# Kernel optimization log

Hardware: AMD Instinct MI355X
Metric: run time of the kernel (lower is better)

The kernel has to match this reference:

```python
import jax, jax.numpy as jnp
import numpy as np
from jax import lax

N_ITER = 50  # entmax-bisect iterations (entmax library default)
DEG = 12    # neighbors per node in global item graph


def entmax_bisect(X, alpha):
    # entmax with per-row alpha, over axis=1. X: [B, L, 1], alpha: [B, 1, 1]
    d = X.shape[1]
    Xa = X * (alpha - 1.0)
    inv = 1.0 / (alpha - 1.0)
    _p = lambda z: jnp.maximum(z, 0.0) ** inv
    max_val = jnp.max(Xa, axis=1, keepdims=True)
    tau_lo = max_val - 1.0                                   # _gp(1, alpha) = 1
    tau_hi = max_val - jnp.power(1.0 / d, alpha - 1.0)       # _gp(1/d, alpha)
    f_lo = jnp.sum(_p(Xa - tau_lo), axis=1, keepdims=True) - 1.0

    def body(i, carry):
        tau_lo, dm, _ = carry
        dm = dm * 0.5
        tau_m = tau_lo + dm
        f_m = jnp.sum(_p(Xa - tau_m), axis=1, keepdims=True) - 1.0
        tau_lo = jnp.where(f_m * f_lo >= 0.0, tau_m, tau_lo)
        return (tau_lo, dm, tau_m)

    tau_lo, dm, tau_m = lax.fori_loop(0, N_ITER, body, (tau_lo, tau_hi - tau_lo, tau_lo))
    p_m = _p(Xa - tau_m)
    return p_m / jnp.sum(p_m, axis=1, keepdims=True)  # ensure_sum_one


def setup_inputs() -> dict:
    key = jax.random.key(0)
    ks = jax.random.split(key, 10)
    B, L, D, N = 1024, 50, 256, 40000
    E = N * DEG
    stdv = 1.0 / np.sqrt(D)
    u = lambda k, shape: jax.random.uniform(k, shape, jnp.float32, -stdv, stdv)

    item_emb = u(ks[0], (N, D)).at[0].set(0.0)  # padding_idx=0
    items = jax.random.randint(ks[1], (B, L), 0, N)
    inputs_seq = jax.random.randint(ks[2], (B, L), 0, N)
    alias_inputs = jax.random.randint(ks[3], (B, L), 0, L)
    target_embedding = jax.random.normal(ks[4], (B, 1, 2 * D), jnp.float32)

    # sparse global item adjacency (row-normalized, DEG neighbors per node)
    adj_rows = jnp.repeat(jnp.arange(N, dtype=jnp.int32), DEG)
    adj_cols = jax.random.randint(ks[5], (E,), 0, N, dtype=jnp.int32)
    adj_vals = jax.random.uniform(ks[6], (E,), jnp.float32) / DEG

    kp = jax.random.split(ks[7], 10)
    return {
        "items": items, "inputs_seq": inputs_seq, "alias_inputs": alias_inputs,
        "target_embedding": target_embedding, "item_emb": item_emb,
        "adj_rows": adj_rows, "adj_cols": adj_cols, "adj_vals": adj_vals,
        "wf_w": u(kp[0], (D, 2 * D)), "wf_b": u(kp[1], (D,)),
        "alphaw_w": u(kp[2], (1, D)), "alphaw_b": u(kp[3], (1,)),
        "at_w0": u(kp[4], (1, D)), "at_w1": u(kp[5], (D, D)),
        "at_w2": u(kp[6], (D, D)), "at_bias": u(kp[7], (D,)),
    }


def reference(items, inputs_seq, alias_inputs, target_embedding, item_emb,
              adj_rows, adj_cols, adj_vals, wf_w, wf_b, alphaw_w, alphaw_b,
              at_w0, at_w1, at_w2, at_bias):
    N = item_emb.shape[0]
    # GlobalItemConv (1 layer): h = (x + adj @ x) / 2 via sparse SpMM
    agg = jax.ops.segment_sum(adj_vals[:, None] * item_emb[adj_cols], adj_rows,
                              num_segments=N)
    graph_embs = (item_emb + agg) * 0.5

    hidden = graph_embs[items]                              # [B, L, D] (dropout: eval)
    target_emb = target_embedding @ wf_w.T + wf_b           # [B, 1, D]

    # get_alpha: sigmoid + 1, then masked_fill(==1 -> 1.00001)
    alpha_ent = jax.nn.sigmoid(target_emb @ alphaw_w.T + alphaw_b) + 1.0  # [B,1,1]
    alpha_ent = jnp.where(alpha_ent == 1.0, 1.00001, alpha_ent)

    # tglobal_attention
    scores = jax.nn.relu(hidden @ at_w1 + target_emb @ at_w2 + at_bias) @ at_w0.T  # [B,L,1]
    attn = entmax_bisect(scores, alpha_ent)                 # sparse softmax over L
    c = jnp.einsum('blo,bld->bod', attn, hidden)[:, 0, :]   # alpha^T @ v, squeeze -> [B,D]

    c = jax.nn.selu(c)
    return c / jnp.linalg.norm(c, axis=-1, keepdims=True)
```

## Files before the change

kernel.cpp:

```cpp
#include <hip/hip_runtime.h>
#include <hip/hip_bf16.h>
#include <math.h>

#define BB 1024
#define LL 50
#define DD 256
#define TWO_D 512
#define NN 40000
#define DEG 12
#define NITER 50

typedef __attribute__((ext_vector_type(8))) short short8;
typedef __attribute__((ext_vector_type(4))) float floatx4;

__device__ __forceinline__ float wave_sum64(float v) {
#pragma unroll
    for (int off = 32; off > 0; off >>= 1) v += __shfl_xor(v, off, 64);
    return v;
}
__device__ __forceinline__ float wave_max64(float v) {
#pragma unroll
    for (int off = 32; off > 0; off >>= 1) v = fmaxf(v, __shfl_xor(v, off, 64));
    return v;
}
__device__ __forceinline__ float dpp_sum64(float v) {
#define DPPADD(ctrl, rm, bm) \
    v += __int_as_float(__builtin_amdgcn_update_dpp(0, __float_as_int(v), ctrl, rm, bm, true))
    DPPADD(0x111, 0xF, 0xF);
    DPPADD(0x112, 0xF, 0xF);
    DPPADD(0x114, 0xF, 0xE);
    DPPADD(0x118, 0xF, 0xC);
    DPPADD(0x142, 0xA, 0xF);
    DPPADD(0x143, 0xC, 0xF);
#undef DPPADD
    return __int_as_float(__builtin_amdgcn_readlane(__float_as_int(v), 63));
}
__device__ __forceinline__ float bf2f(ushort u) {
    union { unsigned int i; float f; } c; c.i = ((unsigned int)u) << 16; return c.f;
}
__device__ __forceinline__ ushort f2bf(float f) {
    __hip_bfloat16 h = __float2bfloat16(f);
    return *(ushort*)&h;
}
__device__ __forceinline__ float hw_exp2(float x) { return __builtin_amdgcn_exp2f(x); }
__device__ __forceinline__ float hw_log2(float x) { return __builtin_amdgcn_logf(x); }

__global__ __launch_bounds__(256) void k_stage1(
    const float* __restrict__ emb, ushort* __restrict__ ebf,
    const int* __restrict__ items, int* __restrict__ flags,
    const float* __restrict__ wf_w, const float* __restrict__ wf_b,
    const float* __restrict__ at_w2, const float* __restrict__ at_bias,
    const float* __restrict__ aw, const float* __restrict__ ab,
    const float* __restrict__ at_w1,
    float* __restrict__ Wc, float* __restrict__ v,
    float* __restrict__ bc, float* __restrict__ c0,
    ushort* __restrict__ w1t)
{
    __shared__ float wcol[DD];
    __shared__ float4 s_p[4][64];
    __shared__ float wred[4];
    __shared__ ushort s_t[4][DD];
    int bid = blockIdx.x;
    int tid = threadIdx.x;

    if (bid < 512) {
        int k = bid;
        int lane = tid & 63, wv = tid >> 6;
        int ng = tid & 63;
        int dq = tid >> 6;

        wcol[tid] = wf_w[tid * TWO_D + k];
        __syncthreads();

        float4 acc = {0.f, 0.f, 0.f, 0.f};
        const float4* w24 = (const float4*)at_w2;
#pragma unroll 8
        for (int d = dq * 64; d < dq * 64 + 64; ++d) {
            float4 w2 = w24[d * 64 + ng];
            float wc = wcol[d];
            acc.x += wc * w2.x; acc.y += wc * w2.y;
            acc.z += wc * w2.z; acc.w += wc * w2.w;
        }
        s_p[dq][ng] = acc;

        float s1 = wcol[tid] * aw[tid];
        s1 = wave_sum64(s1);
        if (lane == 0) wred[wv] = s1;
        __syncthreads();
        if (tid == 0) v[k] = wred[0] + wred[1] + wred[2] + wred[3];

        if (tid < 64) {
            float4 r0 = s_p[0][tid], r1 = s_p[1][tid];
            float4 r2 = s_p[2][tid], r3 = s_p[3][tid];
            float4 rr;
            rr.x = (r0.x + r1.x) + (r2.x + r3.x);
            rr.y = (r0.y + r1.y) + (r2.y + r3.y);
            rr.z = (r0.z + r1.z) + (r2.z + r3.z);
            rr.w = (r0.w + r1.w) + (r2.w + r3.w);
            *(float4*)(Wc + k * DD + tid * 4) = rr;
        }

        if (k < 64) {
            int k0 = k * 4;
#pragma unroll
            for (int j = 0; j < 4; ++j)
                s_t[j][tid] = f2bf(at_w1[(k0 + j) * DD + tid]);
            __syncthreads();
            ushort4 pk;
            pk.x = s_t[0][tid]; pk.y = s_t[1][tid];
            pk.z = s_t[2][tid]; pk.w = s_t[3][tid];
            *(ushort4*)(w1t + tid * DD + k0) = pk;
        }

        if (k == 0) {
            __syncthreads();
            wcol[tid] = wf_b[tid];
            __syncthreads();
            float b[8];
#pragma unroll
            for (int j = 0; j < 8; ++j) b[j] = 0.f;
#pragma unroll 4
            for (int d = 0; d < DD; d += 8) {
#pragma unroll
                for (int j = 0; j < 8; ++j)
                    b[j] += wcol[d + j] * at_w2[(d + j) * DD + tid];
            }
            bc[tid] = at_bias[tid] + ((b[0] + b[1]) + (b[2] + b[3]))
                                   + ((b[4] + b[5]) + (b[6] + b[7]));
            float s2 = wcol[tid] * aw[tid];
            s2 = wave_sum64(s2);
            if (lane == 0) wred[wv] = s2;
            __syncthreads();
            if (tid == 0) c0[0] = wred[0] + wred[1] + wred[2] + wred[3] + ab[0];
        }
    } else if (bid < 712) {
        int i = (bid - 512) * 256 + tid;
        flags[items[i]] = 1;
    } else {
        int base4 = (bid - 712) * (256 * 8) + tid;
        float4 val[8];
#pragma unroll
        for (int j = 0; j < 8; ++j)
            val[j] = *(const float4*)(emb + (size_t)(base4 + j * 256) * 4);
#pragma unroll
        for (int j = 0; j < 8; ++j) {
            ushort4 o;
            o.x = f2bf(val[j].x); o.y = f2bf(val[j].y);
            o.z = f2bf(val[j].z); o.w = f2bf(val[j].w);
            *(ushort4*)(ebf + (size_t)(base4 + j * 256) * 4) = o;
        }
    }
}

__global__ __launch_bounds__(256) void k_stage2(
    const ushort* __restrict__ ebf, const int* __restrict__ adj_cols,
    const float* __restrict__ adj_vals, const int* __restrict__ flags,
    ushort* __restrict__ gbf,
    const float* __restrict__ tgt, const float* __restrict__ Wc,
    const float* __restrict__ bc, const float* __restrict__ v,
    const float* __restrict__ c0, float* __restrict__ t2,
    float* __restrict__ alpha)
{
    __shared__ float x_s[4 * TWO_D];
    int bid = blockIdx.x;
    int tid = threadIdx.x;
    int wv = tid >> 6, lane = tid & 63;

    if (bid < 1024) {
        int t = bid;
        int btile = t >> 2, ntile = t & 3;
        int b0 = btile * 4, n0 = ntile * 64;
        int j = wv;
        for (int i = tid; i < 4 * TWO_D; i += 256) x_s[i] = tgt[b0 * TWO_D + i];
        __syncthreads();

        float acc = bc[n0 + lane];
        const float* xr = x_s + j * TWO_D;
#pragma unroll 8
        for (int k = 0; k < TWO_D; ++k)
            acc += xr[k] * Wc[k * DD + n0 + lane];
        t2[(b0 + j) * DD + n0 + lane] = acc;

        if (ntile == 0) {
            float s = 0.f;
#pragma unroll
            for (int i = 0; i < 8; ++i) s += xr[lane + 64 * i] * v[lane + 64 * i];
            s = wave_sum64(s);
            if (lane == 0) {
                float a = 1.f + 1.f / (1.f + expf(-(s + c0[0])));
                if (a == 1.f) a = 1.00001f;
                alpha[b0 + j] = a;
            }
        }
    } else {
        int n = (bid - 1024) * 4 + wv;
        if (flags[n] != 1) return;
        int colv = 0; float valv = 0.f;
        if (lane < DEG) { colv = adj_cols[n * DEG + lane]; valv = adj_vals[n * DEG + lane]; }
        int cols[DEG]; float vals[DEG];
#pragma unroll
        for (int k = 0; k < DEG; ++k) {
            cols[k] = __builtin_amdgcn_readlane(colv, k);
            vals[k] = __int_as_float(__builtin_amdgcn_readlane(__float_as_int(valv), k));
        }
        ushort4 s = *(const ushort4*)(ebf + (size_t)n * DD + lane * 4);
        ushort4 e[DEG];
#pragma unroll
        for (int k = 0; k < DEG; ++k)
            e[k] = *(const ushort4*)(ebf + (size_t)cols[k] * DD + lane * 4);
        float a0 = bf2f(s.x), a1 = bf2f(s.y), a2 = bf2f(s.z), a3 = bf2f(s.w);
#pragma unroll
        for (int k = 0; k < DEG; ++k) {
            float vv = vals[k];
            a0 += vv * bf2f(e[k].x); a1 += vv * bf2f(e[k].y);
            a2 += vv * bf2f(e[k].z); a3 += vv * bf2f(e[k].w);
        }
        ushort4 o;
        o.x = f2bf(0.5f * a0); o.y = f2bf(0.5f * a1);
        o.z = f2bf(0.5f * a2); o.w = f2bf(0.5f * a3);
        *(ushort4*)(gbf + (size_t)n * DD + lane * 4) = o;
    }
}

__device__ __forceinline__ float pw(float z, float invv) {
    return hw_exp2(invv * hw_log2(z));
}

#define SA_LD 264

__global__ __launch_bounds__(256, 2) void k_fused(
    const int* __restrict__ items, const ushort* __restrict__ gbf,
    const ushort* __restrict__ w1t, const float* __restrict__ t2,
    const float* __restrict__ at_w0, const float* __restrict__ alpha,
    float* __restrict__ out)
{
    __shared__ __align__(16) ushort sA[64 * SA_LD];
    __shared__ __align__(16) ushort sB[256 * 72];
    __shared__ float t2_s[DD];
    __shared__ float sred[64][4];
    __shared__ float scores_s[64];
    __shared__ int s_items[64];
    __shared__ float attn_s[64];
    __shared__ float red[4];

    int b = blockIdx.x;
    int tid = threadIdx.x;
    int lane = tid & 63, wv = tid >> 6;
    int cn = lane & 15, q = lane >> 4;
    int n0 = wv * 64;

    if (tid < 64) {
        int l = (tid < LL) ? tid : 0;
        s_items[tid] = items[b * LL + l];
    }
    t2_s[tid] = t2[b * DD + tid];
    __syncthreads();

#pragma unroll
    for (int it = 0; it < 8; ++it) {
        int i = tid + it * 256;
        int row = i >> 5, ch = i & 31;
        *(uint4*)(sA + row * SA_LD + ch * 8) =
            *(const uint4*)(gbf + (size_t)s_items[row] * DD + ch * 8);
    }

    floatx4 acc[4][4];
#pragma unroll
    for (int mt = 0; mt < 4; ++mt)
#pragma unroll
        for (int nt = 0; nt < 4; ++nt)
            acc[mt][nt] = (floatx4){0.f, 0.f, 0.f, 0.f};

#pragma unroll 1
    for (int kc = 0; kc < 4; ++kc) {
#pragma unroll
        for (int it = 0; it < 8; ++it) {
            int i = tid + it * 256;
            int n = i >> 3, seg = i & 7;
            *(uint4*)(sB + n * 72 + seg * 8) =
                *(const uint4*)(w1t + n * DD + kc * 64 + seg * 8);
        }
        __syncthreads();
#pragma unroll
        for (int ks = 0; ks < 2; ++ks) {
            short8 af[4], bfr[4];
#pragma unroll
            for (int mt = 0; mt < 4; ++mt)
                af[mt] = *(const short8*)(sA + (mt * 16 + cn) * SA_LD + kc * 64 + ks * 32 + q * 8);
#pragma unroll
            for (int nt = 0; nt < 4; ++nt)
                bfr[nt] = *(const short8*)(sB + (n0 + nt * 16 + cn) * 72 + ks * 32 + q * 8);
#pragma unroll
            for (int mt = 0; mt < 4; ++mt)
#pragma unroll
                for (int nt = 0; nt < 4; ++nt)
                    acc[mt][nt] = __builtin_amdgcn_mfma_f32_16x16x32_bf16(
                        af[mt], bfr[nt], acc[mt][nt], 0, 0, 0);
        }
        __syncthreads();
    }

    float w0v[4];
#pragma unroll
    for (int nt = 0; nt < 4; ++nt) w0v[nt] = at_w0[n0 + nt * 16 + cn];
#pragma unroll
    for (int mt = 0; mt < 4; ++mt) {
#pragma unroll
        for (int r = 0; r < 4; ++r) {
            int row = mt * 16 + q * 4 + r;
            float p = 0.f;
#pragma unroll
            for (int nt = 0; nt < 4; ++nt) {
                int col = n0 + nt * 16 + cn;
                float vvv = acc[mt][nt][r] + t2_s[col];
                p += fmaxf(vvv, 0.f) * w0v[nt];
            }
            p += __shfl_xor(p, 1, 64);
            p += __shfl_xor(p, 2, 64);
            p += __shfl_xor(p, 4, 64);
            p += __shfl_xor(p, 8, 64);
            if (cn == 0) sred[row][wv] = p;
        }
    }
    __syncthreads();
    if (tid < 64)
        scores_s[tid] = sred[tid][0] + sred[tid][1] + sred[tid][2] + sred[tid][3];
    __syncthreads();

    if (tid < 64) {
        int l = tid;
        float a = alpha[b];
        float am1 = a - 1.f;
        float invv = 1.f / am1;
        float x = (l < LL) ? scores_s[l] : -__builtin_inff();
        float Xa = x * am1;

        float mx = wave_max64(Xa);
        float tau_lo = mx - 1.f;
        float tau_hi = mx - hw_exp2(am1 * hw_log2(1.f / (float)LL));

        float f_lo = dpp_sum64(pw(fmaxf(Xa - tau_lo, 0.f), invv)) - 1.f;

        float dm = tau_hi - tau_lo;
        float tau_m = tau_lo;
#pragma unroll 1
        for (int it = 0; it < NITER; ++it) {
            dm *= 0.5f;
            tau_m = tau_lo + dm;
            if (tau_m == tau_lo) break;
            float f_m = dpp_sum64(pw(fmaxf(Xa - tau_m, 0.f), invv)) - 1.f;
            if (f_m * f_lo >= 0.f) tau_lo = tau_m;
        }
        float pm = pw(fmaxf(Xa - tau_m, 0.f), invv);
        float s = dpp_sum64(pm);
        if (l < LL) attn_s[l] = pm / s;
    }
    __syncthreads();

    int d = tid;
    float c0_ = 0.f, c1_ = 0.f;
#pragma unroll
    for (int l = 0; l < LL; l += 2) {
        c0_ += attn_s[l]     * bf2f(sA[l * SA_LD + d]);
        c1_ += attn_s[l + 1] * bf2f(sA[(l + 1) * SA_LD + d]);
    }
    float c = c0_ + c1_;

    const float SC = 1.0507009873554805f;
    const float AL = 1.6732632423543772f;
    c = SC * (c > 0.f ? c : AL * expm1f(c));

    float ss = wave_sum64(c * c);
    if (lane == 0) red[wv] = ss;
    __syncthreads();
    float tot = red[0] + red[1] + red[2] + red[3];
    out[b * DD + d] = c / sqrtf(tot);
}

extern "C" void kernel_launch(void* const* d_in, const int* in_sizes, int n_in,
                              void* d_out, int out_size, void* d_ws, size_t ws_size,
                              hipStream_t stream) {
    const int*   items     = (const int*)  d_in[0];
    const float* tgt       = (const float*)d_in[3];
    const float* item_emb  = (const float*)d_in[4];
    const int*   adj_cols  = (const int*)  d_in[6];
    const float* adj_vals  = (const float*)d_in[7];
    const float* wf_w      = (const float*)d_in[8];
    const float* wf_b      = (const float*)d_in[9];
    const float* alphaw_w  = (const float*)d_in[10];
    const float* alphaw_b  = (const float*)d_in[11];
    const float* at_w0     = (const float*)d_in[12];
    const float* at_w1     = (const float*)d_in[13];
    const float* at_w2     = (const float*)d_in[14];
    const float* at_bias   = (const float*)d_in[15];

    const size_t SZ_TAB = (size_t)NN * DD * sizeof(ushort);
    char* ws = (char*)d_ws;
    ushort* gbf = (ushort*)ws;   ws += SZ_TAB;
    ushort* ebf = (ushort*)ws;   ws += SZ_TAB;
    ushort* w1t = (ushort*)ws;   ws += (size_t)DD * DD * sizeof(ushort);
    int*   flags = (int*)ws;     ws += (size_t)NN * sizeof(int);
    float* Wc     = (float*)ws;  ws += (size_t)TWO_D * DD * sizeof(float);
    float* bcv    = (float*)ws;  ws += (size_t)DD * sizeof(float);
    float* vv     = (float*)ws;  ws += (size_t)TWO_D * sizeof(float);
    float* c0v    = (float*)ws;  ws += 16 * sizeof(float);
    float* t2     = (float*)ws;  ws += (size_t)BB * DD * sizeof(float);
    float* alpha  = (float*)ws;  ws += ((size_t)BB + 32) * sizeof(float);
    float* out    = (float*)d_out;

    k_stage1<<<1962, 256, 0, stream>>>(item_emb, ebf, items, flags,
                                       wf_w, wf_b, at_w2, at_bias,
                                       alphaw_w, alphaw_b, at_w1,
                                       Wc, vv, bcv, c0v, w1t);
    k_stage2<<<11024, 256, 0, stream>>>(ebf, adj_cols, adj_vals, flags, gbf,
                                        tgt, Wc, bcv, vv, c0v, t2, alpha);
    k_fused<<<BB, 256, 0, stream>>>(items, gbf, w1t, t2, at_w0, alpha, out);
}
```

Measured before the change: 183.4 us.

## Drop LDS staging in fused attention kernel; load MFMA operands directly from global

The fused kernel no longer stages the gathered hidden rows and the W1 tiles in shared memory. Each wave loads its MFMA fragments straight from global memory, which removes the kc-loop barriers and cuts LDS use so the launch bound can rise from 2 to 4 blocks per CU. The entmax bisection now runs redundantly in all four waves, and the attention weights are broadcast with readlane instead of going through shared memory and a barrier. The cost is that every wave reloads W1 and the hidden rows from global/L2, and the final weighted sum re-gathers those rows from global memory.

```diff
diff --git a/kernel.cpp b/kernel.cpp
--- a/kernel.cpp
+++ b/kernel.cpp
@@ -226,21 +226,15 @@
     return hw_exp2(invv * hw_log2(z));
 }
 
-#define SA_LD 264
-
-__global__ __launch_bounds__(256, 2) void k_fused(
+__global__ __launch_bounds__(256, 4) void k_fused(
     const int* __restrict__ items, const ushort* __restrict__ gbf,
     const ushort* __restrict__ w1t, const float* __restrict__ t2,
     const float* __restrict__ at_w0, const float* __restrict__ alpha,
     float* __restrict__ out)
 {
-    __shared__ __align__(16) ushort sA[64 * SA_LD];
-    __shared__ __align__(16) ushort sB[256 * 72];
     __shared__ float t2_s[DD];
     __shared__ float sred[64][4];
-    __shared__ float scores_s[64];
     __shared__ int s_items[64];
-    __shared__ float attn_s[64];
     __shared__ float red[4];
 
     int b = blockIdx.x;
@@ -256,13 +250,14 @@
     t2_s[tid] = t2[b * DD + tid];
     __syncthreads();
 
-#pragma unroll
-    for (int it = 0; it < 8; ++it) {
-        int i = tid + it * 256;
-        int row = i >> 5, ch = i & 31;
-        *(uint4*)(sA + row * SA_LD + ch * 8) =
-            *(const uint4*)(gbf + (size_t)s_items[row] * DD + ch * 8);
-    }
+    const ushort* arow[4];
+#pragma unroll
+    for (int mt = 0; mt < 4; ++mt)
+        arow[mt] = gbf + (size_t)s_items[mt * 16 + cn] * DD;
+    const ushort* brow[4];
+#pragma unroll
+    for (int nt = 0; nt < 4; ++nt)
+        brow[nt] = w1t + (size_t)(n0 + nt * 16 + cn) * DD;
 
     floatx4 acc[4][4];
 #pragma unroll
@@ -274,22 +269,15 @@
 #pragma unroll 1
     for (int kc = 0; kc < 4; ++kc) {
 #pragma unroll
-        for (int it = 0; it < 8; ++it) {
-            int i = tid + it * 256;
-            int n = i >> 3, seg = i & 7;
-            *(uint4*)(sB + n * 72 + seg * 8) =
-                *(const uint4*)(w1t + n * DD + kc * 64 + seg * 8);
-        }
-        __syncthreads();
-#pragma unroll
         for (int ks = 0; ks < 2; ++ks) {
+            int ko = kc * 64 + ks * 32 + q * 8;
             short8 af[4], bfr[4];
 #pragma unroll
             for (int mt = 0; mt < 4; ++mt)
-                af[mt] = *(const short8*)(sA + (mt * 16 + cn) * SA_LD + kc * 64 + ks * 32 + q * 8);
+                af[mt] = *(const short8*)(arow[mt] + ko);
 #pragma unroll
             for (int nt = 0; nt < 4; ++nt)
-                bfr[nt] = *(const short8*)(sB + (n0 + nt * 16 + cn) * 72 + ks * 32 + q * 8);
+                bfr[nt] = *(const short8*)(brow[nt] + ko);
 #pragma unroll
             for (int mt = 0; mt < 4; ++mt)
 #pragma unroll
@@ -297,7 +285,6 @@
                     acc[mt][nt] = __builtin_amdgcn_mfma_f32_16x16x32_bf16(
                         af[mt], bfr[nt], acc[mt][nt], 0, 0, 0);
         }
-        __syncthreads();
     }
 
     float w0v[4];
@@ -323,48 +310,42 @@
         }
     }
     __syncthreads();
-    if (tid < 64)
-        scores_s[tid] = sred[tid][0] + sred[tid][1] + sred[tid][2] + sred[tid][3];
-    __syncthreads();
-
-    if (tid < 64) {
-        int l = tid;
-        float a = alpha[b];
-        float am1 = a - 1.f;
-        float invv = 1.f / am1;
-        float x = (l < LL) ? scores_s[l] : -__builtin_inff();
-        float Xa = x * am1;
-
-        float mx = wave_max64(Xa);
-        float tau_lo = mx - 1.f;
-        float tau_hi = mx - hw_exp2(am1 * hw_log2(1.f / (float)LL));
-
-        float f_lo = dpp_sum64(pw(fmaxf(Xa - tau_lo, 0.f), invv)) - 1.f;
-
-        float dm = tau_hi - tau_lo;
-        float tau_m = tau_lo;
+
+    float sc = sred[lane][0] + sred[lane][1] + sred[lane][2] + sred[lane][3];
+
+    float a = alpha[b];
+    float am1 = a - 1.f;
+    float invv = 1.f / am1;
+    float x = (lane < LL) ? sc : -__builtin_inff();
+    float Xa = x * am1;
+
+    float mx = wave_max64(Xa);
+    float tau_lo = mx - 1.f;
+    float tau_hi = mx - hw_exp2(am1 * hw_log2(1.f / (float)LL));
+
+    float f_lo = dpp_sum64(pw(fmaxf(Xa - tau_lo, 0.f), invv)) - 1.f;
+
+    float dm = tau_hi - tau_lo;
+    float tau_m = tau_lo;
 #pragma unroll 1
-        for (int it = 0; it < NITER; ++it) {
-            dm *= 0.5f;
-            tau_m = tau_lo + dm;
-            if (tau_m == tau_lo) break;
-            float f_m = dpp_sum64(pw(fmaxf(Xa - tau_m, 0.f), invv)) - 1.f;
-            if (f_m * f_lo >= 0.f) tau_lo = tau_m;
-        }
-        float pm = pw(fmaxf(Xa - tau_m, 0.f), invv);
-        float s = dpp_sum64(pm);
-        if (l < LL) attn_s[l] = pm / s;
-    }
-    __syncthreads();
+    for (int it = 0; it < NITER; ++it) {
+        dm *= 0.5f;
+        tau_m = tau_lo + dm;
+        if (tau_m == tau_lo) break;
+        float f_m = dpp_sum64(pw(fmaxf(Xa - tau_m, 0.f), invv)) - 1.f;
+        if (f_m * f_lo >= 0.f) tau_lo = tau_m;
+    }
+    float pm = pw(fmaxf(Xa - tau_m, 0.f), invv);
+    float sden = dpp_sum64(pm);
+    float pmn = pm / sden;
 
     int d = tid;
-    float c0_ = 0.f, c1_ = 0.f;
-#pragma unroll
-    for (int l = 0; l < LL; l += 2) {
-        c0_ += attn_s[l]     * bf2f(sA[l * SA_LD + d]);
-        c1_ += attn_s[l + 1] * bf2f(sA[(l + 1) * SA_LD + d]);
-    }
-    float c = c0_ + c1_;
+    float c = 0.f;
+#pragma unroll
+    for (int l = 0; l < LL; ++l) {
+        float al = __int_as_float(__builtin_amdgcn_readlane(__float_as_int(pmn), l));
+        c += al * bf2f(gbf[(size_t)s_items[l] * DD + d]);
+    }
 
     const float SC = 1.0507009873554805f;
     const float AL = 1.6732632423543772f;
```

New measurement: 191.6 us (median of 2 runs). +4.4%, slower.
